# Kernel tuning notes

Hardware: AMD Instinct MI355X
Metric: run time of the kernel (lower is better)

The kernel has to match this reference:

```python
import jax, jax.numpy as jnp
import numpy as np

B, S, D, H = 4, 2048, 1024, 16
DK = D // H
WINDOW = 256
GLOBAL = 16
NEG_INF = float(np.finfo(np.float32).min)


def local_window_mask(seq_len, window, global_tokens):
    # 0 where attention allowed, -inf where |i-j| > window and neither i nor j is a global token
    i = jnp.arange(seq_len)[:, None]
    j = jnp.arange(seq_len)[None, :]
    is_global = (i < global_tokens) | (j < global_tokens)
    out_of_window = jnp.abs(i - j) > window
    return jnp.where(out_of_window & ~is_global, NEG_INF, 0.0).astype(jnp.float32)


def setup_inputs() -> dict:
    key = jax.random.key(0)
    ks = jax.random.split(key, 8)
    std = 1.0 / np.sqrt(D)
    return {
        "q": jax.random.normal(ks[0], (B, S, D), jnp.float32),
        "k": jax.random.normal(ks[1], (B, S, D), jnp.float32),
        "v": jax.random.normal(ks[2], (B, S, D), jnp.float32),
        "attn_mask": jnp.zeros((B, S), jnp.float32),
        "wq": jax.random.normal(ks[3], (D, D), jnp.float32) * std,
        "bq": jnp.zeros((D,), jnp.float32),
        "wk": jax.random.normal(ks[4], (D, D), jnp.float32) * std,
        "bk": jnp.zeros((D,), jnp.float32),
        "wv": jax.random.normal(ks[5], (D, D), jnp.float32) * std,
        "bv": jnp.zeros((D,), jnp.float32),
        "wo": jax.random.normal(ks[6], (D, D), jnp.float32) * std,
        "bo": jnp.zeros((D,), jnp.float32),
    }


def reference(q, k, v, attn_mask, wq, bq, wk, bk, wv, bv, wo, bo):
    b, s, d = q.shape
    # projections (x @ W + b)
    Q = (q @ wq + bq).reshape(b, s, H, DK).transpose(0, 2, 1, 3)  # b h s dk
    K = (k @ wk + bk).reshape(b, s, H, DK).transpose(0, 2, 1, 3)
    V = (v @ wv + bv).reshape(b, s, H, DK).transpose(0, 2, 1, 3)

    scale = 1.0 / np.sqrt(DK)
    scores = jnp.einsum("bhqd,bhkd->bhqk", Q, K) * scale  # b h s s
    # additive key mask broadcast over query positions: attn_mask[:, None, None, :]
    scores = scores + attn_mask[:, None, None, :]
    scores = scores + local_window_mask(s, WINDOW, GLOBAL)[None, None, :, :]
    probs = jax.nn.softmax(scores, axis=-1)
    out = jnp.einsum("bhqk,bhkd->bhqd", probs, V)  # b h s dk
    out = out.transpose(0, 2, 1, 3).reshape(b, s, d)
    return out @ wo + bo
```

## Files before the change

kernel.cpp:

```cpp
#include <hip/hip_runtime.h>


#define B_   4
#define S_   2048
#define D_   1024
#define H_   16
#define DK_  64
#define WIN_ 256
#define GLB_ 16

typedef __attribute__((ext_vector_type(8))) short bf16x8;
typedef __attribute__((ext_vector_type(4))) float floatx4;

__device__ __forceinline__ unsigned short f2bf(float x) {
  unsigned u = __float_as_uint(x);
  unsigned r = u + 0x7FFFu + ((u >> 16) & 1u);
  return (unsigned short)(r >> 16);
}
__device__ __forceinline__ float bf2f(unsigned short h) {
  return __uint_as_float(((unsigned)h) << 16);
}
__device__ __forceinline__ void gload_lds16(const void* g, void* l) {
  __builtin_amdgcn_global_load_lds(
      (const __attribute__((address_space(1))) unsigned int*)g,
      (__attribute__((address_space(3))) unsigned int*)l, 16, 0, 0);
}

__global__ void split_bf16(const float* __restrict__ x,
                           unsigned short* __restrict__ hi,
                           unsigned short* __restrict__ lo)
{
  const int i = blockIdx.x * 256 + threadIdx.x;
  const float4 v = ((const float4*)x)[i];
  unsigned short h0 = f2bf(v.x), h1 = f2bf(v.y), h2 = f2bf(v.z), h3 = f2bf(v.w);
  unsigned short l0 = f2bf(v.x - bf2f(h0)), l1 = f2bf(v.y - bf2f(h1));
  unsigned short l2 = f2bf(v.z - bf2f(h2)), l3 = f2bf(v.w - bf2f(h3));
  unsigned long long hp = (unsigned long long)h0 | ((unsigned long long)h1 << 16)
                        | ((unsigned long long)h2 << 32) | ((unsigned long long)h3 << 48);
  unsigned long long lp = (unsigned long long)l0 | ((unsigned long long)l1 << 16)
                        | ((unsigned long long)l2 << 32) | ((unsigned long long)l3 << 48);
  ((unsigned long long*)hi)[i] = hp;
  ((unsigned long long*)lo)[i] = lp;
}

__global__ void wtsplit(const float* __restrict__ W,
                        unsigned short* __restrict__ hiT,
                        unsigned short* __restrict__ loT)
{
  __shared__ float t[32][33];
  const int bx = blockIdx.x * 32;
  const int by = blockIdx.y * 32;
  const int c = threadIdx.x & 31;
  const int r0 = (threadIdx.x >> 5) * 4;
#pragma unroll
  for (int i = 0; i < 4; ++i)
    t[r0 + i][c] = W[(size_t)(by + r0 + i) * 1024 + bx + c];
  __syncthreads();
#pragma unroll
  for (int i = 0; i < 4; ++i) {
    const int r = r0 + i;
    const float val = t[c][r];
    const unsigned short h = f2bf(val);
    hiT[(size_t)(bx + r) * 1024 + by + c] = h;
    loT[(size_t)(bx + r) * 1024 + by + c] = f2bf(val - bf2f(h));
  }
}

__global__ __launch_bounds__(256, 2) void gemm_mfma(
    const unsigned short* __restrict__ Ahi, const unsigned short* __restrict__ Alo,
    const unsigned short* __restrict__ WThi, const unsigned short* __restrict__ WTlo,
    const float* __restrict__ bias, float* __restrict__ Cf,
    unsigned short* __restrict__ Chi, unsigned short* __restrict__ Clo, int mode)
{
  __shared__ unsigned short AsH[4096], AsL[4096], WsH[4096], WsL[4096];
  const int tid = threadIdx.x;
  const int w = tid >> 6, lane = tid & 63;
  const int wr = w >> 1, wc = w & 1;
  const int bm = blockIdx.y * 128, bn = blockIdx.x * 128;
  const int lrow = lane & 15, lk8 = (lane >> 4) * 8;

  floatx4 acc[4][4];
#pragma unroll
  for (int t = 0; t < 4; ++t)
#pragma unroll
    for (int u = 0; u < 4; ++u) acc[t][u] = (floatx4){0.f, 0.f, 0.f, 0.f};

  const unsigned short* gsrc;
  unsigned short* lbase;
  int growbase;
  if      (w == 0) { gsrc = Ahi;  lbase = AsH; growbase = bm; }
  else if (w == 1) { gsrc = Alo;  lbase = AsL; growbase = bm; }
  else if (w == 2) { gsrc = WThi; lbase = WsH; growbase = bn; }
  else             { gsrc = WTlo; lbase = WsL; growbase = bn; }

  for (int k0 = 0; k0 < 1024; k0 += 32) {
    __syncthreads();
#pragma unroll
    for (int g = 0; g < 8; ++g) {
      const unsigned short* gp =
          gsrc + (size_t)(growbase + g * 16 + lrow) * 1024 + k0 + lk8;
      gload_lds16(gp, lbase + g * 512);
    }
    __syncthreads();

    bf16x8 ah[4], al[4], bh[4], bl[4];
#pragma unroll
    for (int t = 0; t < 4; ++t) {
      ah[t] = *(const bf16x8*)&AsH[(wr * 4 + t) * 512 + lane * 8];
      al[t] = *(const bf16x8*)&AsL[(wr * 4 + t) * 512 + lane * 8];
    }
#pragma unroll
    for (int u = 0; u < 4; ++u) {
      bh[u] = *(const bf16x8*)&WsH[(wc * 4 + u) * 512 + lane * 8];
      bl[u] = *(const bf16x8*)&WsL[(wc * 4 + u) * 512 + lane * 8];
    }
#pragma unroll
    for (int t = 0; t < 4; ++t)
#pragma unroll
      for (int u = 0; u < 4; ++u) {
        acc[t][u] = __builtin_amdgcn_mfma_f32_16x16x32_bf16(al[t], bh[u], acc[t][u], 0, 0, 0);
        acc[t][u] = __builtin_amdgcn_mfma_f32_16x16x32_bf16(ah[t], bl[u], acc[t][u], 0, 0, 0);
        acc[t][u] = __builtin_amdgcn_mfma_f32_16x16x32_bf16(ah[t], bh[u], acc[t][u], 0, 0, 0);
      }
  }

  float bs[4];
#pragma unroll
  for (int u = 0; u < 4; ++u) bs[u] = bias[bn + wc * 64 + u * 16 + lrow];

#pragma unroll
  for (int t = 0; t < 4; ++t)
#pragma unroll
    for (int r = 0; r < 4; ++r) {
      const int row = bm + wr * 64 + t * 16 + (lane >> 4) * 4 + r;
#pragma unroll
      for (int u = 0; u < 4; ++u) {
        const int col = bn + wc * 64 + u * 16 + lrow;
        const float val = acc[t][u][r] + bs[u];
        if (mode == 0) {
          Cf[(size_t)row * 1024 + col] = val;
        } else {
          const int bb = row >> 11, s = row & 2047;
          const int hh = col >> 6, dk = col & 63;
          if (mode == 1) {
            const size_t a = ((size_t)(bb * H_ + hh) * S_ + s) * DK_ + dk;
            const unsigned short hv = f2bf(val);
            Chi[a] = hv;
            Clo[a] = f2bf(val - bf2f(hv));
          } else {
            Chi[((size_t)(bb * H_ + hh) * DK_ + dk) * S_ + s] = f2bf(val);
          }
        }
      }
    }
}

__global__ __launch_bounds__(256, 2) void attn_mfma(
    const unsigned short* __restrict__ Qhi, const unsigned short* __restrict__ Qlo,
    const unsigned short* __restrict__ Khi, const unsigned short* __restrict__ Klo,
    const unsigned short* __restrict__ Vt,  const float* __restrict__ amask,
    unsigned short* __restrict__ AOhi, unsigned short* __restrict__ AOlo)
{
  __shared__ unsigned short Pall[4][1024];

  const int tid = threadIdx.x;
  const int w = tid >> 6, lane = tid & 63;
  const int quad = lane >> 4, lm = lane & 15;
  const int strip = blockIdx.x * 4 + w;
  const int h = blockIdx.y, b = blockIdx.z;
  const int i0w = strip * 16;

  const size_t hb = (size_t)(b * H_ + h) * S_ * DK_;
  const unsigned short* Qhih = Qhi + hb;
  const unsigned short* Qloh = Qlo + hb;
  const unsigned short* Khih = Khi + hb;
  const unsigned short* Kloh = Klo + hb;
  const unsigned short* Vth  = Vt  + hb;

  const int myrow = i0w + lm;

  bf16x8 bqh[2], bql[2];
#pragma unroll
  for (int p = 0; p < 2; ++p) {
    const size_t qa = (size_t)myrow * DK_ + p * 32 + quad * 8;
    bqh[p] = *(const bf16x8*)(Qhih + qa);
    bql[p] = *(const bf16x8*)(Qloh + qa);
  }

  floatx4 acc[4];
  float m_i = -1e30f, l_i = 0.f;
#pragma unroll
  for (int u = 0; u < 4; ++u) acc[u] = (floatx4){0.f, 0.f, 0.f, 0.f};

  int t_lo = (i0w - WIN_) >> 6; if (t_lo < 1) t_lo = 1;
  int t_hi = (i0w + 15 + WIN_) >> 6; if (t_hi > 31) t_hi = 31;
  const int nt = (i0w == 0) ? 32 : (t_hi - t_lo + 2);

  unsigned short* Pw = Pall[w];

  for (int it = 0; it < nt; ++it) {
    const int kt = (i0w == 0) ? it : ((it == 0) ? 0 : (t_lo + it - 1));
    const int k0 = kt * 64;

    bf16x8 kh[4][2], kl[4][2];
#pragma unroll
    for (int u = 0; u < 4; ++u)
#pragma unroll
      for (int p = 0; p < 2; ++p) {
        const size_t ka = (size_t)(k0 + u * 16 + lm) * DK_ + p * 32 + quad * 8;
        kh[u][p] = *(const bf16x8*)(Khih + ka);
        kl[u][p] = *(const bf16x8*)(Kloh + ka);
      }
    bf16x8 vt[4][2];
#pragma unroll
    for (int u = 0; u < 4; ++u)
#pragma unroll
      for (int p = 0; p < 2; ++p)
        vt[u][p] = *(const bf16x8*)(Vth + (size_t)(u * 16 + lm) * S_ + k0 + p * 32 + quad * 8);

    floatx4 sc[4];
#pragma unroll
    for (int u = 0; u < 4; ++u) sc[u] = (floatx4){0.f, 0.f, 0.f, 0.f};
#pragma unroll
    for (int u = 0; u < 4; ++u)
#pragma unroll
      for (int p = 0; p < 2; ++p) {
        sc[u] = __builtin_amdgcn_mfma_f32_16x16x32_bf16(kh[u][p], bql[p], sc[u], 0, 0, 0);
        sc[u] = __builtin_amdgcn_mfma_f32_16x16x32_bf16(kl[u][p], bqh[p], sc[u], 0, 0, 0);
        sc[u] = __builtin_amdgcn_mfma_f32_16x16x32_bf16(kh[u][p], bqh[p], sc[u], 0, 0, 0);
      }

    const bool easy = (i0w == 0) ||
                      (kt >= 1 && k0 >= i0w - (WIN_ - 15) && k0 <= i0w + (WIN_ - 63));
    float mx = -1e30f;
    if (easy) {
#pragma unroll
      for (int u = 0; u < 4; ++u) {
        const float4 amv = *(const float4*)(amask + b * S_ + k0 + u * 16 + quad * 4);
        const float amr[4] = {amv.x, amv.y, amv.z, amv.w};
#pragma unroll
        for (int r = 0; r < 4; ++r) {
          const float sv = fmaf(sc[u][r], 0.125f, amr[r]);
          sc[u][r] = sv;
          mx = fmaxf(mx, sv);
        }
      }
    } else {
      const bool iglb = (myrow < GLB_);
#pragma unroll
      for (int u = 0; u < 4; ++u) {
        const float4 amv = *(const float4*)(amask + b * S_ + k0 + u * 16 + quad * 4);
        const float amr[4] = {amv.x, amv.y, amv.z, amv.w};
#pragma unroll
        for (int r = 0; r < 4; ++r) {
          const int j = k0 + u * 16 + quad * 4 + r;
          const int diff = myrow - j;
          const bool ok = (diff <= WIN_ && diff >= -WIN_) || iglb || (j < GLB_);
          const float sv = ok ? fmaf(sc[u][r], 0.125f, amr[r]) : -1e30f;
          sc[u][r] = sv;
          mx = fmaxf(mx, sv);
        }
      }
    }
    mx = fmaxf(mx, __shfl_xor(mx, 16));
    mx = fmaxf(mx, __shfl_xor(mx, 32));

    const float mn = fmaxf(m_i, mx);
    const float alpha = __expf(m_i - mn);
    m_i = mn;
    float rsum = 0.f;
#pragma unroll
    for (int u = 0; u < 4; ++u)
#pragma unroll
      for (int r = 0; r < 4; ++r) {
        const float pv = __expf(sc[u][r] - mn);
        sc[u][r] = pv;
        rsum += pv;
      }
    rsum += __shfl_xor(rsum, 16);
    rsum += __shfl_xor(rsum, 32);
    l_i = l_i * alpha + rsum;
#pragma unroll
    for (int u = 0; u < 4; ++u) {
      acc[u][0] *= alpha; acc[u][1] *= alpha;
      acc[u][2] *= alpha; acc[u][3] *= alpha;
    }

#pragma unroll
    for (int u = 0; u < 4; ++u) {
      const unsigned long long pk =
          (unsigned long long)f2bf(sc[u][0])
        | ((unsigned long long)f2bf(sc[u][1]) << 16)
        | ((unsigned long long)f2bf(sc[u][2]) << 32)
        | ((unsigned long long)f2bf(sc[u][3]) << 48);
      *(unsigned long long*)&Pw[(u * 2 + (quad >> 1)) * 128 + lm * 8 + (quad & 1) * 4] = pk;
    }

#pragma unroll
    for (int p = 0; p < 2; ++p) {
      const bf16x8 pf = *(const bf16x8*)&Pw[p * 512 + lane * 8];
#pragma unroll
      for (int u = 0; u < 4; ++u)
        acc[u] = __builtin_amdgcn_mfma_f32_16x16x32_bf16(vt[u][p], pf, acc[u], 0, 0, 0);
    }
  }

  const float linv = 1.0f / l_i;
  const size_t rowa = (size_t)(b * S_ + myrow) * D_ + h * DK_;
#pragma unroll
  for (int u = 0; u < 4; ++u) {
    float vv[4];
    unsigned short hv[4];
#pragma unroll
    for (int r = 0; r < 4; ++r) { vv[r] = acc[u][r] * linv; hv[r] = f2bf(vv[r]); }
    unsigned long long hp = (unsigned long long)hv[0] | ((unsigned long long)hv[1] << 16)
                          | ((unsigned long long)hv[2] << 32) | ((unsigned long long)hv[3] << 48);
    unsigned long long lp = 0;
#pragma unroll
    for (int r = 0; r < 4; ++r)
      lp |= ((unsigned long long)f2bf(vv[r] - bf2f(hv[r]))) << (16 * r);
    *(unsigned long long*)&AOhi[rowa + u * 16 + quad * 4] = hp;
    *(unsigned long long*)&AOlo[rowa + u * 16 + quad * 4] = lp;
  }
}

#define BM 128
#define BN 128
#define BK 16

__global__ __launch_bounds__(256, 2) void gemm_f32(
    const float* __restrict__ A, const float* __restrict__ W,
    const float* __restrict__ bias, float* __restrict__ C, int mode)
{
  __shared__ float As[BK][BM + 4];
  __shared__ float Bs[BK][BN + 4];
  const int tid = threadIdx.x;
  const int bm = blockIdx.y * BM;
  const int bn = blockIdx.x * BN;
  const int tx = tid & 15;
  const int ty = tid >> 4;
  const int K = 1024, N = 1024;

  float acc[8][8];
#pragma unroll
  for (int i = 0; i < 8; ++i)
#pragma unroll
    for (int j = 0; j < 8; ++j) acc[i][j] = 0.f;

  const int arow = tid >> 2;
  const int acol = (tid & 3) * 4;
  const int brow = tid >> 5;
  const int bcol = (tid & 31) * 4;

  for (int k0 = 0; k0 < K; k0 += BK) {
    float4 a0 = *(const float4*)(A + (size_t)(bm + arow) * K + k0 + acol);
    float4 a1 = *(const float4*)(A + (size_t)(bm + arow + 64) * K + k0 + acol);
    float4 b0 = *(const float4*)(W + (size_t)(k0 + brow) * N + bn + bcol);
    float4 b1 = *(const float4*)(W + (size_t)(k0 + brow + 8) * N + bn + bcol);
    __syncthreads();
    As[acol + 0][arow] = a0.x; As[acol + 1][arow] = a0.y;
    As[acol + 2][arow] = a0.z; As[acol + 3][arow] = a0.w;
    As[acol + 0][arow + 64] = a1.x; As[acol + 1][arow + 64] = a1.y;
    As[acol + 2][arow + 64] = a1.z; As[acol + 3][arow + 64] = a1.w;
    *(float4*)&Bs[brow][bcol]     = b0;
    *(float4*)&Bs[brow + 8][bcol] = b1;
    __syncthreads();
#pragma unroll
    for (int kk = 0; kk < BK; ++kk) {
      float a[8], bb[8];
      float4 t;
      t = *(float4*)&As[kk][ty * 8];     a[0]=t.x; a[1]=t.y; a[2]=t.z; a[3]=t.w;
      t = *(float4*)&As[kk][ty * 8 + 4]; a[4]=t.x; a[5]=t.y; a[6]=t.z; a[7]=t.w;
      t = *(float4*)&Bs[kk][tx * 8];     bb[0]=t.x; bb[1]=t.y; bb[2]=t.z; bb[3]=t.w;
      t = *(float4*)&Bs[kk][tx * 8 + 4]; bb[4]=t.x; bb[5]=t.y; bb[6]=t.z; bb[7]=t.w;
#pragma unroll
      for (int i = 0; i < 8; ++i)
#pragma unroll
        for (int j = 0; j < 8; ++j)
          acc[i][j] = fmaf(a[i], bb[j], acc[i][j]);
    }
  }

  const float4 bias0 = *(const float4*)(bias + bn + tx * 8);
  const float4 bias1 = *(const float4*)(bias + bn + tx * 8 + 4);
  if (mode == 0) {
#pragma unroll
    for (int i = 0; i < 8; ++i) {
      const int m = bm + ty * 8 + i;
      float* dst = C + (size_t)m * 1024 + bn + tx * 8;
      *(float4*)dst = make_float4(acc[i][0] + bias0.x, acc[i][1] + bias0.y,
                                  acc[i][2] + bias0.z, acc[i][3] + bias0.w);
      *(float4*)(dst + 4) = make_float4(acc[i][4] + bias1.x, acc[i][5] + bias1.y,
                                        acc[i][6] + bias1.z, acc[i][7] + bias1.w);
    }
  } else {
    const int ncol = bn + tx * 8;
    const int h  = ncol >> 6;
    const int dk = ncol & 63;
#pragma unroll
    for (int i = 0; i < 8; ++i) {
      const int m = bm + ty * 8 + i;
      const int bb2 = m >> 11;
      const int s  = m & 2047;
      float* dst = C + ((size_t)(bb2 * H_ + h) * S_ + s) * DK_ + dk;
      *(float4*)dst = make_float4(acc[i][0] + bias0.x, acc[i][1] + bias0.y,
                                  acc[i][2] + bias0.z, acc[i][3] + bias0.w);
      *(float4*)(dst + 4) = make_float4(acc[i][4] + bias1.x, acc[i][5] + bias1.y,
                                        acc[i][6] + bias1.z, acc[i][7] + bias1.w);
    }
  }
}

__global__ __launch_bounds__(256, 2) void attn_v3(
    const float* __restrict__ Qp, const float* __restrict__ Kp,
    const float* __restrict__ Vp, const float* __restrict__ amask,
    float* __restrict__ AO)
{
  __shared__ float Qs[64][68], Ks[64][68], Vs[64][68], Ps[64][68];

  const int tid = threadIdx.x;
  const int qt = blockIdx.x;
  const int h  = blockIdx.y;
  const int b  = blockIdx.z;
  const int i0 = qt * 64;
  const int tr = tid >> 4;
  const int tc = tid & 15;

  const size_t head_off = (size_t)(b * H_ + h) * S_ * DK_;
  const float* Qh = Qp + head_off;
  const float* Kh = Kp + head_off;
  const float* Vh = Vp + head_off;

#pragma unroll
  for (int r = 0; r < 4; ++r) {
    const int f = tid + r * 256;
    const int row = f >> 4, col = (f & 15) * 4;
    *(float4*)&Qs[row][col] = *(const float4*)(Qh + (size_t)(i0 + row) * DK_ + col);
  }

  float m_i[4], l_i[4];
  float4 acc[4];
#pragma unroll
  for (int i = 0; i < 4; ++i) {
    m_i[i] = -1e30f; l_i[i] = 0.f;
    acc[i] = make_float4(0.f, 0.f, 0.f, 0.f);
  }

  int start, t_lo, t_hi;
  if (qt == 0) { start = 0; t_lo = 0; t_hi = 31; }
  else {
    start = -1;
    t_lo = qt - 4 < 1 ? 1 : qt - 4;
    t_hi = qt + 4 > 31 ? 31 : qt + 4;
  }

  for (int tt = start; tt <= t_hi; ++tt) {
    if (tt >= 0 && tt < t_lo) continue;
    const int kt = (tt < 0) ? 0 : tt;
    const int k0 = kt * 64;

    __syncthreads();
#pragma unroll
    for (int r = 0; r < 4; ++r) {
      const int f = tid + r * 256;
      const int row = f >> 4, col = (f & 15) * 4;
      *(float4*)&Ks[row][col] = *(const float4*)(Kh + (size_t)(k0 + row) * DK_ + col);
      *(float4*)&Vs[row][col] = *(const float4*)(Vh + (size_t)(k0 + row) * DK_ + col);
    }
    __syncthreads();

    float am[4];
#pragma unroll
    for (int u = 0; u < 4; ++u) am[u] = amask[b * S_ + k0 + tc + 16 * u];

    float s[4][4];
#pragma unroll
    for (int i = 0; i < 4; ++i)
#pragma unroll
      for (int u = 0; u < 4; ++u) s[i][u] = 0.f;
#pragma unroll
    for (int d4 = 0; d4 < 16; ++d4) {
      const float4 k0v = *(float4*)&Ks[tc     ][d4 * 4];
      const float4 k1v = *(float4*)&Ks[tc + 16][d4 * 4];
      const float4 k2v = *(float4*)&Ks[tc + 32][d4 * 4];
      const float4 k3v = *(float4*)&Ks[tc + 48][d4 * 4];
#pragma unroll
      for (int i = 0; i < 4; ++i) {
        const float4 q = *(float4*)&Qs[tr * 4 + i][d4 * 4];
        s[i][0] += q.x*k0v.x + q.y*k0v.y + q.z*k0v.z + q.w*k0v.w;
        s[i][1] += q.x*k1v.x + q.y*k1v.y + q.z*k1v.z + q.w*k1v.w;
        s[i][2] += q.x*k2v.x + q.y*k2v.y + q.z*k2v.z + q.w*k2v.w;
        s[i][3] += q.x*k3v.x + q.y*k3v.y + q.z*k3v.z + q.w*k3v.w;
      }
    }

#pragma unroll
    for (int i = 0; i < 4; ++i) {
      const int irow = i0 + tr * 4 + i;
#pragma unroll
      for (int u = 0; u < 4; ++u) {
        const int j = k0 + tc + 16 * u;
        const int diff = irow - j;
        const bool allowed = (diff <= WIN_ && diff >= -WIN_) || (irow < GLB_) || (j < GLB_);
        s[i][u] = allowed ? fmaf(s[i][u], 0.125f, am[u]) : -1e30f;
      }
    }

    float mt[4];
#pragma unroll
    for (int i = 0; i < 4; ++i)
      mt[i] = fmaxf(fmaxf(s[i][0], s[i][1]), fmaxf(s[i][2], s[i][3]));
#pragma unroll
    for (int st = 1; st <= 8; st <<= 1)
#pragma unroll
      for (int i = 0; i < 4; ++i)
        mt[i] = fmaxf(mt[i], __shfl_xor(mt[i], st));

    float alpha[4], rs[4];
#pragma unroll
    for (int i = 0; i < 4; ++i) {
      const float mn = fmaxf(m_i[i], mt[i]);
      alpha[i] = __expf(m_i[i] - mn);
      m_i[i] = mn;
      float r = 0.f;
#pragma unroll
      for (int u = 0; u < 4; ++u) {
        s[i][u] = __expf(s[i][u] - mn);
        r += s[i][u];
      }
      rs[i] = r;
    }
#pragma unroll
    for (int st = 1; st <= 8; st <<= 1)
#pragma unroll
      for (int i = 0; i < 4; ++i)
        rs[i] += __shfl_xor(rs[i], st);
#pragma unroll
    for (int i = 0; i < 4; ++i) {
      l_i[i] = l_i[i] * alpha[i] + rs[i];
      acc[i].x *= alpha[i]; acc[i].y *= alpha[i];
      acc[i].z *= alpha[i]; acc[i].w *= alpha[i];
    }

#pragma unroll
    for (int u = 0; u < 4; ++u)
      *(float4*)&Ps[tc + 16 * u][tr * 4] =
          make_float4(s[0][u], s[1][u], s[2][u], s[3][u]);
    __syncthreads();

#pragma unroll 4
    for (int j = 0; j < 64; ++j) {
      const float4 p4 = *(float4*)&Ps[j][tr * 4];
      const float4 v4 = *(float4*)&Vs[j][tc * 4];
      acc[0].x = fmaf(p4.x, v4.x, acc[0].x); acc[0].y = fmaf(p4.x, v4.y, acc[0].y);
      acc[0].z = fmaf(p4.x, v4.z, acc[0].z); acc[0].w = fmaf(p4.x, v4.w, acc[0].w);
      acc[1].x = fmaf(p4.y, v4.x, acc[1].x); acc[1].y = fmaf(p4.y, v4.y, acc[1].y);
      acc[1].z = fmaf(p4.y, v4.z, acc[1].z); acc[1].w = fmaf(p4.y, v4.w, acc[1].w);
      acc[2].x = fmaf(p4.z, v4.x, acc[2].x); acc[2].y = fmaf(p4.z, v4.y, acc[2].y);
      acc[2].z = fmaf(p4.z, v4.z, acc[2].z); acc[2].w = fmaf(p4.z, v4.w, acc[2].w);
      acc[3].x = fmaf(p4.w, v4.x, acc[3].x); acc[3].y = fmaf(p4.w, v4.y, acc[3].y);
      acc[3].z = fmaf(p4.w, v4.z, acc[3].z); acc[3].w = fmaf(p4.w, v4.w, acc[3].w);
    }
  }

#pragma unroll
  for (int i = 0; i < 4; ++i) {
    const float linv = 1.0f / l_i[i];
    const int row = i0 + tr * 4 + i;
    float* dst = AO + ((size_t)b * S_ + row) * D_ + h * DK_ + tc * 4;
    *(float4*)dst = make_float4(acc[i].x * linv, acc[i].y * linv,
                                acc[i].z * linv, acc[i].w * linv);
  }
}

extern "C" void kernel_launch(void* const* d_in, const int* in_sizes, int n_in,
                              void* d_out, int out_size, void* d_ws, size_t ws_size,
                              hipStream_t stream) {
  const float* q  = (const float*)d_in[0];
  const float* k  = (const float*)d_in[1];
  const float* v  = (const float*)d_in[2];
  const float* am = (const float*)d_in[3];
  const float* wq = (const float*)d_in[4];
  const float* bq = (const float*)d_in[5];
  const float* wk = (const float*)d_in[6];
  const float* bk = (const float*)d_in[7];
  const float* wv = (const float*)d_in[8];
  const float* bv = (const float*)d_in[9];
  const float* wo = (const float*)d_in[10];
  const float* bo = (const float*)d_in[11];
  float* out = (float*)d_out;

  const size_t PER = (size_t)B_ * H_ * S_ * DK_;
  const size_t NEED = 138412032;

  if (ws_size >= NEED) {
    unsigned short* us = (unsigned short*)d_ws;
    unsigned short* ACTh = us;
    unsigned short* ACTl = us + PER;
    unsigned short* Qhi  = us + 2 * PER;
    unsigned short* Qlo  = us + 3 * PER;
    unsigned short* Khi  = us + 4 * PER;
    unsigned short* Klo  = us + 5 * PER;
    unsigned short* Vtp  = us + 6 * PER;
    unsigned short* WHI  = us + 7 * PER;
    unsigned short* WLO  = WHI + 1048576;

    const int sgrid = (int)(PER / 4 / 256);
    dim3 wgrid(32, 32);
    dim3 ggrid(8, 64);

    split_bf16<<<sgrid, 256, 0, stream>>>(q, ACTh, ACTl);
    wtsplit<<<wgrid, 256, 0, stream>>>(wq, WHI, WLO);
    gemm_mfma<<<ggrid, 256, 0, stream>>>(ACTh, ACTl, WHI, WLO, bq, nullptr, Qhi, Qlo, 1);

    split_bf16<<<sgrid, 256, 0, stream>>>(k, ACTh, ACTl);
    wtsplit<<<wgrid, 256, 0, stream>>>(wk, WHI, WLO);
    gemm_mfma<<<ggrid, 256, 0, stream>>>(ACTh, ACTl, WHI, WLO, bk, nullptr, Khi, Klo, 1);

    split_bf16<<<sgrid, 256, 0, stream>>>(v, ACTh, ACTl);
    wtsplit<<<wgrid, 256, 0, stream>>>(wv, WHI, WLO);
    gemm_mfma<<<ggrid, 256, 0, stream>>>(ACTh, ACTl, WHI, WLO, bv, nullptr, Vtp, nullptr, 2);

    attn_mfma<<<dim3(32, H_, B_), 256, 0, stream>>>(
        Qhi, Qlo, Khi, Klo, Vtp, am, ACTh, ACTl);

    wtsplit<<<wgrid, 256, 0, stream>>>(wo, WHI, WLO);
    gemm_mfma<<<ggrid, 256, 0, stream>>>(ACTh, ACTl, WHI, WLO, bo, out, nullptr, nullptr, 0);
  } else {
    float* Qp = (float*)d_ws;
    float* Kp = Qp + PER;
    float* Vp = Kp + PER;
    float* AOf = Vp + PER;
    dim3 gg(D_ / BN, (B_ * S_) / BM);
    gemm_f32<<<gg, 256, 0, stream>>>(q, wq, bq, Qp, 1);
    gemm_f32<<<gg, 256, 0, stream>>>(k, wk, bk, Kp, 1);
    gemm_f32<<<gg, 256, 0, stream>>>(v, wv, bv, Vp, 1);
    attn_v3<<<dim3(S_ / 64, H_, B_), 256, 0, stream>>>(Qp, Kp, Vp, am, AOf);
    gemm_f32<<<gg, 256, 0, stream>>>(AOf, wo, bo, out, 0);
  }
}
```

Baseline: 751.3 us.

## Process two query fragments per wave and drop online softmax max tracking

Each wave now computes 32 query rows (two 16-row fragments) and shares the K and V tile loads across both, halving the grid and the K/V load traffic per query row. The running-max online softmax is replaced by a direct exp of the clamped score with the sum reduced once at the end, which removes the per-tile max shuffles and accumulator rescaling. This raises register pressure and halves the number of blocks. It also gives up overflow protection for large scores, since scores above 60 are clamped rather than normalised.

```diff
diff --git a/kernel.cpp b/kernel.cpp
--- a/kernel.cpp
+++ b/kernel.cpp
@@ -161,14 +161,14 @@
     const unsigned short* __restrict__ Vt,  const float* __restrict__ amask,
     unsigned short* __restrict__ AOhi, unsigned short* __restrict__ AOlo)
 {
-  __shared__ unsigned short Pall[4][1024];
+  __shared__ unsigned short Pall[4][2][1024];
 
   const int tid = threadIdx.x;
   const int w = tid >> 6, lane = tid & 63;
   const int quad = lane >> 4, lm = lane & 15;
   const int strip = blockIdx.x * 4 + w;
   const int h = blockIdx.y, b = blockIdx.z;
-  const int i0w = strip * 16;
+  const int i0w = strip * 32;
 
   const size_t hb = (size_t)(b * H_ + h) * S_ * DK_;
   const unsigned short* Qhih = Qhi + hb;
@@ -177,150 +177,148 @@
   const unsigned short* Kloh = Klo + hb;
   const unsigned short* Vth  = Vt  + hb;
 
-  const int myrow = i0w + lm;
-
-  bf16x8 bqh[2], bql[2];
-#pragma unroll
-  for (int p = 0; p < 2; ++p) {
-    const size_t qa = (size_t)myrow * DK_ + p * 32 + quad * 8;
-    bqh[p] = *(const bf16x8*)(Qhih + qa);
-    bql[p] = *(const bf16x8*)(Qloh + qa);
-  }
-
-  floatx4 acc[4];
-  float m_i = -1e30f, l_i = 0.f;
-#pragma unroll
-  for (int u = 0; u < 4; ++u) acc[u] = (floatx4){0.f, 0.f, 0.f, 0.f};
+  bf16x8 bqh[2][2], bql[2][2];
+#pragma unroll
+  for (int f = 0; f < 2; ++f)
+#pragma unroll
+    for (int p = 0; p < 2; ++p) {
+      const size_t qa = (size_t)(i0w + f * 16 + lm) * DK_ + p * 32 + quad * 8;
+      bqh[f][p] = *(const bf16x8*)(Qhih + qa);
+      bql[f][p] = *(const bf16x8*)(Qloh + qa);
+    }
+
+  floatx4 acc[2][4];
+  float l_i[2] = {0.f, 0.f};
+#pragma unroll
+  for (int f = 0; f < 2; ++f)
+#pragma unroll
+    for (int u = 0; u < 4; ++u) acc[f][u] = (floatx4){0.f, 0.f, 0.f, 0.f};
 
   int t_lo = (i0w - WIN_) >> 6; if (t_lo < 1) t_lo = 1;
-  int t_hi = (i0w + 15 + WIN_) >> 6; if (t_hi > 31) t_hi = 31;
+  int t_hi = (i0w + 31 + WIN_) >> 6; if (t_hi > 31) t_hi = 31;
   const int nt = (i0w == 0) ? 32 : (t_hi - t_lo + 2);
-
-  unsigned short* Pw = Pall[w];
 
   for (int it = 0; it < nt; ++it) {
     const int kt = (i0w == 0) ? it : ((it == 0) ? 0 : (t_lo + it - 1));
     const int k0 = kt * 64;
 
-    bf16x8 kh[4][2], kl[4][2];
+    bf16x8 vt[4][2];
 #pragma unroll
     for (int u = 0; u < 4; ++u)
+#pragma unroll
+      for (int p = 0; p < 2; ++p)
+        vt[u][p] = *(const bf16x8*)(Vth + (size_t)(u * 16 + lm) * S_ + k0 + p * 32 + quad * 8);
+
+    floatx4 sc[2][4];
+#pragma unroll
+    for (int f = 0; f < 2; ++f)
+#pragma unroll
+      for (int u = 0; u < 4; ++u) sc[f][u] = (floatx4){0.f, 0.f, 0.f, 0.f};
+#pragma unroll
+    for (int u = 0; u < 4; ++u) {
+      bf16x8 kh[2], kl[2];
 #pragma unroll
       for (int p = 0; p < 2; ++p) {
         const size_t ka = (size_t)(k0 + u * 16 + lm) * DK_ + p * 32 + quad * 8;
-        kh[u][p] = *(const bf16x8*)(Khih + ka);
-        kl[u][p] = *(const bf16x8*)(Kloh + ka);
-      }
-    bf16x8 vt[4][2];
-#pragma unroll
-    for (int u = 0; u < 4; ++u)
-#pragma unroll
-      for (int p = 0; p < 2; ++p)
-        vt[u][p] = *(const bf16x8*)(Vth + (size_t)(u * 16 + lm) * S_ + k0 + p * 32 + quad * 8);
-
-    floatx4 sc[4];
-#pragma unroll
-    for (int u = 0; u < 4; ++u) sc[u] = (floatx4){0.f, 0.f, 0.f, 0.f};
-#pragma unroll
-    for (int u = 0; u < 4; ++u)
-#pragma unroll
-      for (int p = 0; p < 2; ++p) {
-        sc[u] = __builtin_amdgcn_mfma_f32_16x16x32_bf16(kh[u][p], bql[p], sc[u], 0, 0, 0);
-        sc[u] = __builtin_amdgcn_mfma_f32_16x16x32_bf16(kl[u][p], bqh[p], sc[u], 0, 0, 0);
-        sc[u] = __builtin_amdgcn_mfma_f32_16x16x32_bf16(kh[u][p], bqh[p], sc[u], 0, 0, 0);
-      }
-
-    const bool easy = (i0w == 0) ||
-                      (kt >= 1 && k0 >= i0w - (WIN_ - 15) && k0 <= i0w + (WIN_ - 63));
-    float mx = -1e30f;
-    if (easy) {
+        kh[p] = *(const bf16x8*)(Khih + ka);
+        kl[p] = *(const bf16x8*)(Kloh + ka);
+      }
+#pragma unroll
+      for (int f = 0; f < 2; ++f)
+#pragma unroll
+        for (int p = 0; p < 2; ++p) {
+          sc[f][u] = __builtin_amdgcn_mfma_f32_16x16x32_bf16(kh[p], bql[f][p], sc[f][u], 0, 0, 0);
+          sc[f][u] = __builtin_amdgcn_mfma_f32_16x16x32_bf16(kl[p], bqh[f][p], sc[f][u], 0, 0, 0);
+          sc[f][u] = __builtin_amdgcn_mfma_f32_16x16x32_bf16(kh[p], bqh[f][p], sc[f][u], 0, 0, 0);
+        }
+    }
+
+    bool easy;
+    if (i0w == 0) easy = (k0 + 63 <= GLB_ + WIN_);
+    else          easy = (kt >= 1) && (k0 >= i0w + 31 - WIN_) && (k0 + 63 <= i0w + WIN_);
+
+#pragma unroll
+    for (int u = 0; u < 4; ++u) {
+      const float4 amv = *(const float4*)(amask + b * S_ + k0 + u * 16 + quad * 4);
+      const float amr[4] = {amv.x, amv.y, amv.z, amv.w};
+      if (easy) {
+#pragma unroll
+        for (int f = 0; f < 2; ++f)
+#pragma unroll
+          for (int r = 0; r < 4; ++r) {
+            const float p = __expf(fminf(fmaf(sc[f][u][r], 0.125f, amr[r]), 60.f));
+            sc[f][u][r] = p;
+            l_i[f] += p;
+          }
+      } else {
+#pragma unroll
+        for (int f = 0; f < 2; ++f) {
+          const int i = i0w + f * 16 + lm;
+          const bool iglb = (i < GLB_);
+#pragma unroll
+          for (int r = 0; r < 4; ++r) {
+            const int j = k0 + u * 16 + quad * 4 + r;
+            const int diff = i - j;
+            const bool ok = (diff <= WIN_ && diff >= -WIN_) || iglb || (j < GLB_);
+            float p = 0.f;
+            if (ok) p = __expf(fminf(fmaf(sc[f][u][r], 0.125f, amr[r]), 60.f));
+            sc[f][u][r] = p;
+            l_i[f] += p;
+          }
+        }
+      }
+    }
+
+#pragma unroll
+    for (int f = 0; f < 2; ++f)
 #pragma unroll
       for (int u = 0; u < 4; ++u) {
-        const float4 amv = *(const float4*)(amask + b * S_ + k0 + u * 16 + quad * 4);
-        const float amr[4] = {amv.x, amv.y, amv.z, amv.w};
-#pragma unroll
-        for (int r = 0; r < 4; ++r) {
-          const float sv = fmaf(sc[u][r], 0.125f, amr[r]);
-          sc[u][r] = sv;
-          mx = fmaxf(mx, sv);
-        }
-      }
-    } else {
-      const bool iglb = (myrow < GLB_);
-#pragma unroll
-      for (int u = 0; u < 4; ++u) {
-        const float4 amv = *(const float4*)(amask + b * S_ + k0 + u * 16 + quad * 4);
-        const float amr[4] = {amv.x, amv.y, amv.z, amv.w};
-#pragma unroll
-        for (int r = 0; r < 4; ++r) {
-          const int j = k0 + u * 16 + quad * 4 + r;
-          const int diff = myrow - j;
-          const bool ok = (diff <= WIN_ && diff >= -WIN_) || iglb || (j < GLB_);
-          const float sv = ok ? fmaf(sc[u][r], 0.125f, amr[r]) : -1e30f;
-          sc[u][r] = sv;
-          mx = fmaxf(mx, sv);
-        }
-      }
-    }
-    mx = fmaxf(mx, __shfl_xor(mx, 16));
-    mx = fmaxf(mx, __shfl_xor(mx, 32));
-
-    const float mn = fmaxf(m_i, mx);
-    const float alpha = __expf(m_i - mn);
-    m_i = mn;
-    float rsum = 0.f;
-#pragma unroll
-    for (int u = 0; u < 4; ++u)
-#pragma unroll
-      for (int r = 0; r < 4; ++r) {
-        const float pv = __expf(sc[u][r] - mn);
-        sc[u][r] = pv;
-        rsum += pv;
-      }
-    rsum += __shfl_xor(rsum, 16);
-    rsum += __shfl_xor(rsum, 32);
-    l_i = l_i * alpha + rsum;
+        const unsigned long long pk =
+            (unsigned long long)f2bf(sc[f][u][0])
+          | ((unsigned long long)f2bf(sc[f][u][1]) << 16)
+          | ((unsigned long long)f2bf(sc[f][u][2]) << 32)
+          | ((unsigned long long)f2bf(sc[f][u][3]) << 48);
+        *(unsigned long long*)&Pall[w][f][(u * 2 + (quad >> 1)) * 128 + lm * 8 + (quad & 1) * 4] = pk;
+      }
+
+#pragma unroll
+    for (int p = 0; p < 2; ++p) {
+#pragma unroll
+      for (int f = 0; f < 2; ++f) {
+        const bf16x8 pf = *(const bf16x8*)&Pall[w][f][p * 512 + lane * 8];
+#pragma unroll
+        for (int u = 0; u < 4; ++u)
+          acc[f][u] = __builtin_amdgcn_mfma_f32_16x16x32_bf16(vt[u][p], pf, acc[f][u], 0, 0, 0);
+      }
+    }
+  }
+
+#pragma unroll
+  for (int f = 0; f < 2; ++f) {
+    l_i[f] += __shfl_xor(l_i[f], 16);
+    l_i[f] += __shfl_xor(l_i[f], 32);
+  }
+
+#pragma unroll
+  for (int f = 0; f < 2; ++f) {
+    const float linv = 1.0f / l_i[f];
+    const int myrow = i0w + f * 16 + lm;
+    const size_t rowa = (size_t)(b * S_ + myrow) * D_ + h * DK_;
 #pragma unroll
     for (int u = 0; u < 4; ++u) {
-      acc[u][0] *= alpha; acc[u][1] *= alpha;
-      acc[u][2] *= alpha; acc[u][3] *= alpha;
-    }
-
-#pragma unroll
-    for (int u = 0; u < 4; ++u) {
-      const unsigned long long pk =
-          (unsigned long long)f2bf(sc[u][0])
-        | ((unsigned long long)f2bf(sc[u][1]) << 16)
-        | ((unsigned long long)f2bf(sc[u][2]) << 32)
-        | ((unsigned long long)f2bf(sc[u][3]) << 48);
-      *(unsigned long long*)&Pw[(u * 2 + (quad >> 1)) * 128 + lm * 8 + (quad & 1) * 4] = pk;
-    }
-
-#pragma unroll
-    for (int p = 0; p < 2; ++p) {
-      const bf16x8 pf = *(const bf16x8*)&Pw[p * 512 + lane * 8];
-#pragma unroll
-      for (int u = 0; u < 4; ++u)
-        acc[u] = __builtin_amdgcn_mfma_f32_16x16x32_bf16(vt[u][p], pf, acc[u], 0, 0, 0);
-    }
-  }
-
-  const float linv = 1.0f / l_i;
-  const size_t rowa = (size_t)(b * S_ + myrow) * D_ + h * DK_;
-#pragma unroll
-  for (int u = 0; u < 4; ++u) {
-    float vv[4];
-    unsigned short hv[4];
-#pragma unroll
-    for (int r = 0; r < 4; ++r) { vv[r] = acc[u][r] * linv; hv[r] = f2bf(vv[r]); }
-    unsigned long long hp = (unsigned long long)hv[0] | ((unsigned long long)hv[1] << 16)
-                          | ((unsigned long long)hv[2] << 32) | ((unsigned long long)hv[3] << 48);
-    unsigned long long lp = 0;
-#pragma unroll
-    for (int r = 0; r < 4; ++r)
-      lp |= ((unsigned long long)f2bf(vv[r] - bf2f(hv[r]))) << (16 * r);
-    *(unsigned long long*)&AOhi[rowa + u * 16 + quad * 4] = hp;
-    *(unsigned long long*)&AOlo[rowa + u * 16 + quad * 4] = lp;
+      float vv[4];
+      unsigned short hv[4];
+#pragma unroll
+      for (int r = 0; r < 4; ++r) { vv[r] = acc[f][u][r] * linv; hv[r] = f2bf(vv[r]); }
+      unsigned long long hp = (unsigned long long)hv[0] | ((unsigned long long)hv[1] << 16)
+                            | ((unsigned long long)hv[2] << 32) | ((unsigned long long)hv[3] << 48);
+      unsigned long long lp = 0;
+#pragma unroll
+      for (int r = 0; r < 4; ++r)
+        lp |= ((unsigned long long)f2bf(vv[r] - bf2f(hv[r]))) << (16 * r);
+      *(unsigned long long*)&AOhi[rowa + u * 16 + quad * 4] = hp;
+      *(unsigned long long*)&AOlo[rowa + u * 16 + quad * 4] = lp;
+    }
   }
 }
 
@@ -621,7 +619,7 @@
     wtsplit<<<wgrid, 256, 0, stream>>>(wv, WHI, WLO);
     gemm_mfma<<<ggrid, 256, 0, stream>>>(ACTh, ACTl, WHI, WLO, bv, nullptr, Vtp, nullptr, 2);
 
-    attn_mfma<<<dim3(32, H_, B_), 256, 0, stream>>>(
+    attn_mfma<<<dim3(16, H_, B_), 256, 0, stream>>>(
         Qhi, Qlo, Khi, Klo, Vtp, am, ACTh, ACTl);
 
     wtsplit<<<wgrid, 256, 0, stream>>>(wo, WHI, WLO);
```

New measurement: 697.9 us. 1.08x faster.
